# Performance work log

Measured on AMD Instinct MI355X. Metric: run time of the kernel, lower is better.

Reference implementation:

```python
import jax, jax.numpy as jnp
import numpy as np
import math

B, S, D = 2, 1024, 1024
H = 16
HD = D // H
E = 8
DFF = 4096
EPS = 1e-5


def _ln(x, g, b):
    m = jnp.mean(x, axis=-1, keepdims=True)
    v = jnp.mean((x - m) ** 2, axis=-1, keepdims=True)
    return (x - m) / jnp.sqrt(v + EPS) * g + b


def setup_inputs() -> dict:
    key = jax.random.key(0)
    ks = jax.random.split(key, 16)
    s = 0.02
    inp = {
        'src': jax.random.normal(ks[0], (B, S, D), jnp.float32),
        'qw': jax.random.normal(ks[1], (D, D), jnp.float32) * s,
        'kw': jax.random.normal(ks[2], (D, D), jnp.float32) * s,
        'vw': jax.random.normal(ks[3], (D, D), jnp.float32) * s,
        'ow': jax.random.normal(ks[4], (D, D), jnp.float32) * s,
        'gate_w': jax.random.normal(ks[5], (D, D), jnp.float32) * s,
        'gate_b': jax.random.normal(ks[6], (D,), jnp.float32) * s,
        'scale_w': jax.random.normal(ks[7], (H, HD), jnp.float32) * s,
        'n1_g': jnp.ones((D,), jnp.float32),
        'n1_b': jnp.zeros((D,), jnp.float32),
        'n2_g': jnp.ones((D,), jnp.float32),
        'n2_b': jnp.zeros((D,), jnp.float32),
        'moe_gate_w': jax.random.normal(ks[8], (D, E), jnp.float32) * s,
        'moe_gate_b': jnp.zeros((E,), jnp.float32),
        'w1': jax.random.normal(ks[9], (E, D, DFF), jnp.float32) * s,
        'b1': jnp.zeros((E, DFF), jnp.float32),
        'ln_g': jnp.ones((E, DFF), jnp.float32),
        'ln_b': jnp.zeros((E, DFF), jnp.float32),
        'w2': jax.random.normal(ks[10], (E, DFF, D), jnp.float32) * s,
        'b2': jnp.zeros((E, D), jnp.float32),
        'res_scale': jnp.ones((E,), jnp.float32),
    }
    return inp


def _forward(src, qw, kw, vw, ow, gate_w, gate_b, scale_w, n1_g, n1_b, n2_g, n2_b,
             moe_gate_w, moe_gate_b, w1, b1, ln_g, ln_b, w2, b2, res_scale):
    # ---- MemoAttention (non-flash path, eval: no dropout, no mask) ----
    q = (src @ qw).reshape(B, S, H, HD).transpose(0, 2, 1, 3)  # [B,H,S,HD]
    k = (src @ kw).reshape(B, S, H, HD).transpose(0, 2, 1, 3)
    v = (src @ vw).reshape(B, S, H, HD).transpose(0, 2, 1, 3)
    scores = jnp.einsum('bhqd,bhkd->bhqk', q, k) / math.sqrt(HD)
    # dynamic per-(head,query) scale gate
    scale = jax.nn.sigmoid(jnp.einsum('bhsd,hd->bhs', q, scale_w)) * 2.0
    scores = scores * scale[..., None]
    attn = jax.nn.softmax(scores, axis=-1)
    out = jnp.einsum('bhqk,bhkd->bhqd', attn, v)
    out = out.transpose(0, 2, 1, 3).reshape(B, S, D)
    gate = jax.nn.sigmoid(out @ gate_w + gate_b)
    attn_out = (out * gate) @ ow

    x = _ln(src + attn_out, n1_g, n1_b)

    # ---- MoE FFN (top-2 routing; eval: no gate noise; capacity never exceeded) ----
    xf = x.reshape(-1, D)                      # [T, D]
    T = xf.shape[0]
    logits = xf @ moe_gate_w + moe_gate_b      # [T, E]
    top_v, top_i = jax.lax.top_k(logits, 2)
    # NB: original sums BOTH top-k softmax weights per token (== 1.0), and the
    wsum = jnp.sum(jax.nn.softmax(top_v, axis=-1), axis=-1)   # [T] (== 1)
    e_sel = jnp.max(top_i, axis=-1)                           # [T]
    # dense per-expert FFN on all tokens, then per-token select (masked compute)
    h = jnp.einsum('td,edf->etf', xf, w1) + b1[:, None, :]    # [E,T,DFF]
    h = _ln(h, ln_g[:, None, :], ln_b[:, None, :])
    h = jax.nn.gelu(h, approximate=False)                     # torch nn.GELU (erf)
    y = jnp.einsum('etf,efd->etd', h, w2) + b2[:, None, :]    # [E,T,D]
    y = y * res_scale[:, None, None] + xf[None]
    sel = jnp.take_along_axis(y, e_sel[None, :, None], axis=0)[0]  # [T,D]
    moe_out = (sel * wsum[:, None]).reshape(B, S, D)

    return _ln(x + moe_out, n2_g, n2_b)


def reference(src, qw, kw, vw, ow, gate_w, gate_b, scale_w, n1_g, n1_b, n2_g, n2_b,
              moe_gate_w, moe_gate_b, w1, b1, ln_g, ln_b, w2, b2, res_scale):
    return _forward(src, qw, kw, vw, ow, gate_w, gate_b, scale_w, n1_g, n1_b,
                    n2_g, n2_b, moe_gate_w, moe_gate_b, w1, b1, ln_g, ln_b,
                    w2, b2, res_scale)
```

## Files before the change

### kernel.cpp

```cpp
#include <hip/hip_runtime.h>
#include <math.h>

#define TOK    2048
#define DMODEL 1024
#define NHEAD  16
#define HDIM   64
#define NEXP   8
#define DFFN   4096

typedef unsigned short u16;
typedef __attribute__((ext_vector_type(8))) short short8;
typedef __attribute__((ext_vector_type(4))) float floatx4;

__device__ __forceinline__ float sigmoidf_(float x) { return 1.f / (1.f + __expf(-x)); }

__device__ __forceinline__ u16 f2bf(float f) {
  union { float f; unsigned u; } v; v.f = f;
  unsigned r = v.u + 0x7FFFu + ((v.u >> 16) & 1u);
  return (u16)(r >> 16);
}
__device__ __forceinline__ float bf2f(u16 h) {
  union { unsigned u; float f; } v; v.u = ((unsigned)h) << 16; return v.f;
}

__device__ __forceinline__ void gload16(const void* g, void* l) {
  __builtin_amdgcn_global_load_lds((const __attribute__((address_space(1))) void*)g,
                                   (__attribute__((address_space(3))) void*)l, 16, 0, 0);
}

__device__ __forceinline__ float blockReduceSum256(float val) {
  __shared__ float ws_[4];
  #pragma unroll
  for (int off = 32; off; off >>= 1) val += __shfl_down(val, off);
  int lane = threadIdx.x & 63, w = threadIdx.x >> 6;
  if (lane == 0) ws_[w] = val;
  __syncthreads();
  float r = ws_[0] + ws_[1] + ws_[2] + ws_[3];
  __syncthreads();
  return r;
}

__global__ __launch_bounds__(256) void split_kernel(
    const float* __restrict__ X, u16* __restrict__ Hi, u16* __restrict__ Lo) {
  const int i = blockIdx.x * 256 + threadIdx.x;
  const float4 v = ((const float4*)X)[i];
  const float f[4] = {v.x, v.y, v.z, v.w};
  union { u16 s[4]; uint2 u; } h, l;
  #pragma unroll
  for (int j = 0; j < 4; ++j) {
    h.s[j] = f2bf(f[j]);
    l.s[j] = f2bf(f[j] - bf2f(h.s[j]));
  }
  ((uint2*)Hi)[i] = h.u;
  ((uint2*)Lo)[i] = l.u;
}

template<bool LO>
__global__ __launch_bounds__(256) void wt_conv_kernel(
    const float* __restrict__ W, u16* __restrict__ Whi, u16* __restrict__ Wlo,
    int K, int N) {
  const size_t z = blockIdx.z;
  W   += z * (size_t)K * N;
  Whi += z * (size_t)K * N;
  if (LO) Wlo += z * (size_t)K * N;
  __shared__ float tile[32][33];
  const int n0 = blockIdx.x * 32, k0 = blockIdx.y * 32;
  const int r = threadIdx.x >> 3, c4 = (threadIdx.x & 7) * 4;
  const float4 v = *(const float4*)&W[(size_t)(k0 + r) * N + n0 + c4];
  tile[r][c4+0] = v.x; tile[r][c4+1] = v.y; tile[r][c4+2] = v.z; tile[r][c4+3] = v.w;
  __syncthreads();
  union { u16 s[4]; uint2 u; } h, l;
  #pragma unroll
  for (int j = 0; j < 4; ++j) {
    const float f = tile[c4 + j][r];
    h.s[j] = f2bf(f);
    if (LO) l.s[j] = f2bf(f - bf2f(h.s[j]));
  }
  *(uint2*)&Whi[(size_t)(n0 + r) * K + k0 + c4] = h.u;
  if (LO) *(uint2*)&Wlo[(size_t)(n0 + r) * K + k0 + c4] = l.u;
}

__global__ __launch_bounds__(256) void wt3_conv_kernel(
    const float* __restrict__ Q, const float* __restrict__ Kw,
    const float* __restrict__ V, u16* __restrict__ Whi, u16* __restrict__ Wlo) {
  const int zz = blockIdx.z >> 5;
  const float* W = (zz == 0) ? Q : (zz == 1) ? Kw : V;
  u16* Whi_ = Whi + (size_t)zz * DMODEL * DMODEL;
  u16* Wlo_ = Wlo + (size_t)zz * DMODEL * DMODEL;
  __shared__ float tile[32][33];
  const int n0 = blockIdx.x * 32, k0 = (blockIdx.z & 31) * 32;
  const int r = threadIdx.x >> 3, c4 = (threadIdx.x & 7) * 4;
  const float4 v = *(const float4*)&W[(size_t)(k0 + r) * DMODEL + n0 + c4];
  tile[r][c4+0] = v.x; tile[r][c4+1] = v.y; tile[r][c4+2] = v.z; tile[r][c4+3] = v.w;
  __syncthreads();
  union { u16 s[4]; uint2 u; } h, l;
  #pragma unroll
  for (int j = 0; j < 4; ++j) {
    const float f = tile[c4 + j][r];
    h.s[j] = f2bf(f);
    l.s[j] = f2bf(f - bf2f(h.s[j]));
  }
  *(uint2*)&Whi_[(size_t)(n0 + r) * DMODEL + k0 + c4] = h.u;
  *(uint2*)&Wlo_[(size_t)(n0 + r) * DMODEL + k0 + c4] = l.u;
}

template<int EPI, int TN>
__global__ __launch_bounds__(256, TN == 64 ? 3 : 2) void gemm_split_kernel(
    const u16* __restrict__ Ahi, const u16* __restrict__ Alo,
    const u16* __restrict__ Whi, const u16* __restrict__ Wlo,
    const float* __restrict__ bias, const float* __restrict__ mul,
    float* __restrict__ Cf, u16* __restrict__ Chi, u16* __restrict__ Clo,
    u16* __restrict__ Vth, u16* __restrict__ Vtl,
    int M, int N, int K) {
  constexpr int NF = TN / 32;
  __shared__ u16 Ah[128*64], Al[128*64], Bh[TN*64], Bl[TN*64];
  const int tid = threadIdx.x;
  const int lane = tid & 63, wave = tid >> 6;
  const int row0 = blockIdx.y * 128, col0 = blockIdx.x * TN;
  const int wm = (wave & 1) * 64, wn = (wave >> 1) * (TN / 2);
  const int mr = tid >> 3;
  const int ksrc = (tid & 7) ^ ((tid >> 3) & 7);
  const floatx4 zero = {0.f, 0.f, 0.f, 0.f};
  floatx4 acc[4][NF];
  #pragma unroll
  for (int i = 0; i < 4; ++i)
    #pragma unroll
    for (int j = 0; j < NF; ++j) acc[i][j] = zero;

  for (int k0 = 0; k0 < K; k0 += 64) {
    __syncthreads();
    #pragma unroll
    for (int p = 0; p < 4; ++p) {
      const size_t ga = (size_t)(row0 + p * 32 + mr) * K + (k0 + ksrc * 8);
      const size_t off = (size_t)(p * 256 + wave * 64) * 16;
      gload16(Ahi + ga, (char*)Ah + off);
      gload16(Alo + ga, (char*)Al + off);
    }
    #pragma unroll
    for (int p = 0; p < NF; ++p) {
      const size_t gb = (size_t)(col0 + p * 32 + mr) * K + (k0 + ksrc * 8);
      const size_t off = (size_t)(p * 256 + wave * 64) * 16;
      gload16(Whi + gb, (char*)Bh + off);
      gload16(Wlo + gb, (char*)Bl + off);
    }
    __syncthreads();
    #pragma unroll
    for (int kk = 0; kk < 2; ++kk) {
      short8 ah[4], al[4], bh[NF], bl[NF];
      #pragma unroll
      for (int i = 0; i < 4; ++i) {
        const int ml = wm + i * 16 + (lane & 15);
        const int cm = (kk * 4 + (lane >> 4)) ^ (ml & 7);
        ah[i] = *(const short8*)&Ah[ml * 64 + cm * 8];
        al[i] = *(const short8*)&Al[ml * 64 + cm * 8];
      }
      #pragma unroll
      for (int j = 0; j < NF; ++j) {
        const int nl = wn + j * 16 + (lane & 15);
        const int cn = (kk * 4 + (lane >> 4)) ^ (nl & 7);
        bh[j] = *(const short8*)&Bh[nl * 64 + cn * 8];
        bl[j] = *(const short8*)&Bl[nl * 64 + cn * 8];
      }
      #pragma unroll
      for (int i = 0; i < 4; ++i)
        #pragma unroll
        for (int j = 0; j < NF; ++j) {
          acc[i][j] = __builtin_amdgcn_mfma_f32_16x16x32_bf16(ah[i], bh[j], acc[i][j], 0, 0, 0);
          acc[i][j] = __builtin_amdgcn_mfma_f32_16x16x32_bf16(al[i], bh[j], acc[i][j], 0, 0, 0);
          acc[i][j] = __builtin_amdgcn_mfma_f32_16x16x32_bf16(ah[i], bl[j], acc[i][j], 0, 0, 0);
        }
    }
  }
  const int cl = lane & 15, quad = lane >> 4;
  if (EPI == 2 && col0 >= 2048) {
    #pragma unroll
    for (int i = 0; i < 4; ++i)
      #pragma unroll
      for (int j = 0; j < NF; ++j) {
        const int dg = col0 + wn + j * 16 + cl - 2048;
        const int bh_ = dg >> 6, d = dg & 63;
        const int row = row0 + wm + i * 16 + quad * 4;
        const int b = row >> 10, t0 = row & 1023;
        union { u16 s[4]; uint2 u; } hh, ll;
        #pragma unroll
        for (int r = 0; r < 4; ++r) {
          const float v = acc[i][j][r];
          hh.s[r] = f2bf(v);
          ll.s[r] = f2bf(v - bf2f(hh.s[r]));
        }
        const size_t base = ((size_t)(b * 16 + bh_) * 64 + d) * 1024 + t0;
        *(uint2*)&Vth[base] = hh.u;
        *(uint2*)&Vtl[base] = ll.u;
      }
    return;
  }
  #pragma unroll
  for (int i = 0; i < 4; ++i)
    #pragma unroll
    for (int j = 0; j < NF; ++j) {
      const int col = col0 + wn + j * 16 + cl;
      #pragma unroll
      for (int r = 0; r < 4; ++r) {
        const int row = row0 + wm + i * 16 + quad * 4 + r;
        const float v = acc[i][j][r];
        if (EPI == 0) {
          Cf[(size_t)row * N + col] = v;
        } else if (EPI == 1) {
          const float s = sigmoidf_(v + bias[col]);
          const float g = s * mul[(size_t)row * N + col];
          const u16 hh = f2bf(g);
          Chi[(size_t)row * N + col] = hh;
          Clo[(size_t)row * N + col] = f2bf(g - bf2f(hh));
        } else {
          const u16 hh = f2bf(v);
          Chi[(size_t)row * N + col] = hh;
          Clo[(size_t)row * N + col] = f2bf(v - bf2f(hh));
        }
      }
    }
}

template<int EPI, int TN>
__global__ __launch_bounds__(256, TN == 64 ? 4 : 3) void gemm_moe_kernel(
    const u16* __restrict__ A, const u16* __restrict__ Wt,
    const float* __restrict__ bias,
    const int* __restrict__ perm, const int* __restrict__ offs,
    const int* __restrict__ counts,
    u16* __restrict__ Hout, float* __restrict__ P0, float* __restrict__ P1,
    int N, int K, int e_base) {
  constexpr int NF = TN / 32;
  const int z = blockIdx.z;
  const int ez = (EPI == 0) ? z : (z & 3);
  const int ks = (EPI == 0) ? 0 : (z >> 2);
  const int e = e_base + ez;
  const int ne = counts[e];
  const int tm = blockIdx.y;
  if (tm * 128 >= ne) return;
  const int kbeg = (EPI == 0) ? 0 : ks * (K >> 1);
  const int kend = (EPI == 0) ? K : kbeg + (K >> 1);
  __shared__ u16 As_[128*64], Bs_[TN*64];
  __shared__ int toks[128];
  const int tid = threadIdx.x;
  if (tid < 128) {
    const int idx = tm * 128 + tid;
    toks[tid] = perm[offs[e] + (idx < ne ? idx : 0)];
  }
  __syncthreads();
  const int lane = tid & 63, wave = tid >> 6;
  const int wm = (wave & 1) * 64, wn = (wave >> 1) * (TN / 2);
  const int mr = tid >> 3;
  const int ksrc = (tid & 7) ^ ((tid >> 3) & 7);
  size_t abase[4];
  #pragma unroll
  for (int p = 0; p < 4; ++p) abase[p] = (size_t)toks[p * 32 + mr] * K;
  const u16* We = Wt + (size_t)ez * N * K;
  const int col0 = blockIdx.x * TN;
  const floatx4 zero = {0.f, 0.f, 0.f, 0.f};
  floatx4 acc[4][NF];
  #pragma unroll
  for (int i = 0; i < 4; ++i)
    #pragma unroll
    for (int j = 0; j < NF; ++j) acc[i][j] = zero;

  for (int k0 = kbeg; k0 < kend; k0 += 64) {
    __syncthreads();
    #pragma unroll
    for (int p = 0; p < 4; ++p) {
      const size_t off = (size_t)(p * 256 + wave * 64) * 16;
      gload16(A + abase[p] + (k0 + ksrc * 8), (char*)As_ + off);
    }
    #pragma unroll
    for (int p = 0; p < NF; ++p) {
      const size_t off = (size_t)(p * 256 + wave * 64) * 16;
      gload16(We + (size_t)(col0 + p * 32 + mr) * K + (k0 + ksrc * 8), (char*)Bs_ + off);
    }
    __syncthreads();
    #pragma unroll
    for (int kk = 0; kk < 2; ++kk) {
      short8 a[4], b[NF];
      #pragma unroll
      for (int i = 0; i < 4; ++i) {
        const int ml = wm + i * 16 + (lane & 15);
        const int cm = (kk * 4 + (lane >> 4)) ^ (ml & 7);
        a[i] = *(const short8*)&As_[ml * 64 + cm * 8];
      }
      #pragma unroll
      for (int j = 0; j < NF; ++j) {
        const int nl = wn + j * 16 + (lane & 15);
        const int cn = (kk * 4 + (lane >> 4)) ^ (nl & 7);
        b[j] = *(const short8*)&Bs_[nl * 64 + cn * 8];
      }
      #pragma unroll
      for (int i = 0; i < 4; ++i)
        #pragma unroll
        for (int j = 0; j < NF; ++j)
          acc[i][j] = __builtin_amdgcn_mfma_f32_16x16x32_bf16(a[i], b[j], acc[i][j], 0, 0, 0);
    }
  }
  const int cl = lane & 15, quad = lane >> 4;
  float* Pp = (EPI == 1) ? (ks ? P1 : P0) : nullptr;
  #pragma unroll
  for (int i = 0; i < 4; ++i)
    #pragma unroll
    for (int j = 0; j < NF; ++j) {
      const int col = col0 + wn + j * 16 + cl;
      #pragma unroll
      for (int r = 0; r < 4; ++r) {
        const int rl = wm + i * 16 + quad * 4 + r;
        if (tm * 128 + rl < ne) {
          const int tok = toks[rl];
          if (EPI == 0)
            Hout[(size_t)tok * N + col] = f2bf(acc[i][j][r] + bias[(size_t)e * N + col]);
          else
            Pp[(size_t)tok * N + col] = acc[i][j][r];
        }
      }
    }
}

__global__ __launch_bounds__(512, 2) void attn_mfma_kernel(
    const u16* __restrict__ QKh, const u16* __restrict__ QKl,
    const u16* __restrict__ Vth, const u16* __restrict__ Vtl,
    const float* __restrict__ scale_w,
    float* __restrict__ AOf, u16* __restrict__ AOh, u16* __restrict__ AOl) {
  const int qt = blockIdx.x, h = blockIdx.y, b = blockIdx.z;
  __shared__ u16 Kh[64*64], Kl[64*64], Vh[64*64], Vl[64*64];
  __shared__ u16 Ph[8][16*40], Pl[8][16*40];
  const int tid = threadIdx.x, lane = tid & 63, wave = tid >> 6;
  const int i15 = lane & 15, quad = lane >> 4;
  const floatx4 zero = {0.f, 0.f, 0.f, 0.f};

  short8 qh[2], ql[2];
  const size_t qrow = ((size_t)b * 1024 + qt * 128 + wave * 16 + i15) * 3072 + h * 64;
  #pragma unroll
  for (int kk = 0; kk < 2; ++kk) {
    qh[kk] = *(const short8*)&QKh[qrow + kk * 32 + quad * 8];
    ql[kk] = *(const short8*)&QKl[qrow + kk * 32 + quad * 8];
  }
  float dot = 0.f;
  #pragma unroll
  for (int kk = 0; kk < 2; ++kk)
    #pragma unroll
    for (int j = 0; j < 8; ++j) {
      const float sw = scale_w[h * 64 + kk * 32 + quad * 8 + j];
      dot += (bf2f((u16)qh[kk][j]) + bf2f((u16)ql[kk][j])) * sw;
    }
  dot += __shfl_xor(dot, 16);
  dot += __shfl_xor(dot, 32);
  const float g = 2.f * sigmoidf_(dot) * 0.125f;
  float stot[4];
  #pragma unroll
  for (int r = 0; r < 4; ++r) stot[r] = __shfl(g, (lane >> 4) * 4 + r);

  float m_r[4], l_r[4];
  floatx4 Of[4];
  #pragma unroll
  for (int r = 0; r < 4; ++r) { m_r[r] = -1e30f; l_r[r] = 0.f; }
  #pragma unroll
  for (int f = 0; f < 4; ++f) Of[f] = zero;
  u16* PhW = Ph[wave];
  u16* PlW = Pl[wave];

  const int sr = tid >> 3;
  const int sc = ((tid & 7) ^ (sr & 7)) * 8;
  for (int kt = 0; kt < 16; ++kt) {
    __syncthreads();
    {
      const size_t off = (size_t)wave * 1024;
      const size_t kg = ((size_t)b * 1024 + kt * 64 + sr) * 3072 + 1024 + h * 64 + sc;
      gload16(QKh + kg, (char*)Kh + off);
      gload16(QKl + kg, (char*)Kl + off);
      const size_t vg = ((size_t)(b * 16 + h) * 64 + sr) * 1024 + kt * 64 + sc;
      gload16(Vth + vg, (char*)Vh + off);
      gload16(Vtl + vg, (char*)Vl + off);
    }
    __syncthreads();
    float pm[4][4];
    #pragma unroll
    for (int jn = 0; jn < 4; ++jn) {
      floatx4 a = zero;
      #pragma unroll
      for (int kk = 0; kk < 2; ++kk) {
        const int n = jn * 16 + i15;
        const int ch = ((kk * 4 + quad) ^ (n & 7)) * 8;
        const short8 bh = *(const short8*)&Kh[n * 64 + ch];
        const short8 bl = *(const short8*)&Kl[n * 64 + ch];
        a = __builtin_amdgcn_mfma_f32_16x16x32_bf16(qh[kk], bh, a, 0, 0, 0);
        a = __builtin_amdgcn_mfma_f32_16x16x32_bf16(ql[kk], bh, a, 0, 0, 0);
        a = __builtin_amdgcn_mfma_f32_16x16x32_bf16(qh[kk], bl, a, 0, 0, 0);
      }
      #pragma unroll
      for (int r = 0; r < 4; ++r) pm[jn][r] = a[r] * stot[r];
    }
    float alpha[4];
    #pragma unroll
    for (int r = 0; r < 4; ++r) {
      float mx = fmaxf(fmaxf(pm[0][r], pm[1][r]), fmaxf(pm[2][r], pm[3][r]));
      mx = fmaxf(mx, __shfl_xor(mx, 1));
      mx = fmaxf(mx, __shfl_xor(mx, 2));
      mx = fmaxf(mx, __shfl_xor(mx, 4));
      mx = fmaxf(mx, __shfl_xor(mx, 8));
      const float mn = fmaxf(m_r[r], mx);
      alpha[r] = __expf(m_r[r] - mn);
      m_r[r] = mn;
      float rs = 0.f;
      #pragma unroll
      for (int jn = 0; jn < 4; ++jn) { pm[jn][r] = __expf(pm[jn][r] - mn); rs += pm[jn][r]; }
      rs += __shfl_xor(rs, 1);
      rs += __shfl_xor(rs, 2);
      rs += __shfl_xor(rs, 4);
      rs += __shfl_xor(rs, 8);
      l_r[r] = l_r[r] * alpha[r] + rs;
    }
    #pragma unroll
    for (int f = 0; f < 4; ++f)
      #pragma unroll
      for (int r = 0; r < 4; ++r) Of[f][r] *= alpha[r];
    #pragma unroll
    for (int kk = 0; kk < 2; ++kk) {
      #pragma unroll
      for (int jj = 0; jj < 2; ++jj) {
        const int jn = kk * 2 + jj;
        #pragma unroll
        for (int r = 0; r < 4; ++r) {
          const int a = (quad * 4 + r) * 40 + jj * 16 + i15;
          const u16 hh = f2bf(pm[jn][r]);
          PhW[a] = hh;
          PlW[a] = f2bf(pm[jn][r] - bf2f(hh));
        }
      }
      const short8 pah = *(const short8*)&PhW[i15 * 40 + quad * 8];
      const short8 pal = *(const short8*)&PlW[i15 * 40 + quad * 8];
      #pragma unroll
      for (int f = 0; f < 4; ++f) {
        const int d = f * 16 + i15;
        const int ch = ((kk * 4 + quad) ^ (d & 7)) * 8;
        const short8 vbh = *(const short8*)&Vh[d * 64 + ch];
        const short8 vbl = *(const short8*)&Vl[d * 64 + ch];
        Of[f] = __builtin_amdgcn_mfma_f32_16x16x32_bf16(pah, vbh, Of[f], 0, 0, 0);
        Of[f] = __builtin_amdgcn_mfma_f32_16x16x32_bf16(pal, vbh, Of[f], 0, 0, 0);
        Of[f] = __builtin_amdgcn_mfma_f32_16x16x32_bf16(pah, vbl, Of[f], 0, 0, 0);
      }
    }
  }
  float inv[4];
  #pragma unroll
  for (int r = 0; r < 4; ++r) inv[r] = 1.f / l_r[r];
  #pragma unroll
  for (int f = 0; f < 4; ++f)
    #pragma unroll
    for (int r = 0; r < 4; ++r) {
      const size_t row = (size_t)b * 1024 + qt * 128 + wave * 16 + quad * 4 + r;
      const int col = h * 64 + f * 16 + i15;
      const float val = Of[f][r] * inv[r];
      AOf[row * 1024 + col] = val;
      const u16 hh = f2bf(val);
      AOh[row * 1024 + col] = hh;
      AOl[row * 1024 + col] = f2bf(val - bf2f(hh));
    }
}

template<bool BF>
__global__ __launch_bounds__(256) void ln_add_kernel(
    const float* __restrict__ A, const float* __restrict__ Bp,
    const float* __restrict__ g, const float* __restrict__ beta,
    float* __restrict__ outf, u16* __restrict__ outh) {
  int t = blockIdx.x, tid = threadIdx.x;
  const float* a = A + (size_t)t * DMODEL;
  const float* b = Bp + (size_t)t * DMODEL;
  float v[4]; float s = 0.f;
  #pragma unroll
  for (int i = 0; i < 4; ++i) { int d = tid + i*256; v[i] = a[d] + b[d]; s += v[i]; }
  s = blockReduceSum256(s);
  float mean = s * (1.f/1024.f);
  float q = 0.f;
  #pragma unroll
  for (int i = 0; i < 4; ++i) { float df = v[i]-mean; q += df*df; }
  q = blockReduceSum256(q);
  float rstd = rsqrtf(q*(1.f/1024.f) + 1e-5f);
  #pragma unroll
  for (int i = 0; i < 4; ++i) {
    int d = tid + i*256;
    float val = (v[i]-mean)*rstd*g[d] + beta[d];
    outf[(size_t)t*DMODEL + d] = val;
    if (BF) outh[(size_t)t*DMODEL + d] = f2bf(val);
  }
}

__global__ __launch_bounds__(256) void ln_final_kernel(
    const float* __restrict__ X, const float* __restrict__ P0,
    const float* __restrict__ P1, const float* __restrict__ B2,
    const float* __restrict__ rsv, const int* __restrict__ e_sel,
    const float* __restrict__ g, const float* __restrict__ beta,
    float* __restrict__ out) {
  int t = blockIdx.x, tid = threadIdx.x;
  const int e = e_sel[t];
  const float rse = rsv[e];
  const float* b2e = B2 + (size_t)e * DMODEL;
  const int d0 = tid * 4;
  const size_t base = (size_t)t * DMODEL + d0;
  const float4 xv = *(const float4*)&X[base];
  const float4 p0v = *(const float4*)&P0[base];
  const float4 p1v = *(const float4*)&P1[base];
  const float4 bv = *(const float4*)&b2e[d0];
  float v[4]; float s = 0.f;
  v[0] = 2.f*xv.x + (p0v.x + p1v.x + bv.x) * rse;
  v[1] = 2.f*xv.y + (p0v.y + p1v.y + bv.y) * rse;
  v[2] = 2.f*xv.z + (p0v.z + p1v.z + bv.z) * rse;
  v[3] = 2.f*xv.w + (p0v.w + p1v.w + bv.w) * rse;
  s = v[0] + v[1] + v[2] + v[3];
  s = blockReduceSum256(s);
  float mean = s * (1.f/1024.f);
  float q = 0.f;
  #pragma unroll
  for (int i = 0; i < 4; ++i) { float df = v[i]-mean; q += df*df; }
  q = blockReduceSum256(q);
  float rstd = rsqrtf(q*(1.f/1024.f) + 1e-5f);
  const float4 g4 = *(const float4*)&g[d0];
  const float4 be4 = *(const float4*)&beta[d0];
  float4 o;
  o.x = (v[0]-mean)*rstd*g4.x + be4.x;
  o.y = (v[1]-mean)*rstd*g4.y + be4.y;
  o.z = (v[2]-mean)*rstd*g4.z + be4.z;
  o.w = (v[3]-mean)*rstd*g4.w + be4.w;
  *(float4*)&out[base] = o;
}

__global__ __launch_bounds__(256) void moe_gate_kernel(
    const float* __restrict__ X, const float* __restrict__ gw,
    const float* __restrict__ gb, int* __restrict__ e_sel) {
  int wave = threadIdx.x >> 6, lane = threadIdx.x & 63;
  int token = blockIdx.x * 4 + wave;
  const float* x = X + (size_t)token * DMODEL;
  float acc[NEXP] = {};
  for (int d = lane; d < DMODEL; d += 64) {
    float xv = x[d];
    const float* gr = gw + (size_t)d * NEXP;
    #pragma unroll
    for (int e = 0; e < NEXP; ++e) acc[e] += xv * gr[e];
  }
  #pragma unroll
  for (int e = 0; e < NEXP; ++e) {
    #pragma unroll
    for (int off = 32; off; off >>= 1) acc[e] += __shfl_down(acc[e], off);
  }
  if (lane == 0) {
    float lg[NEXP];
    #pragma unroll
    for (int e = 0; e < NEXP; ++e) lg[e] = acc[e] + gb[e];
    int i1 = 0;
    for (int e = 1; e < NEXP; ++e) if (lg[e] > lg[i1]) i1 = e;
    int i2 = -1;
    for (int e = 0; e < NEXP; ++e) {
      if (e == i1) continue;
      if (i2 < 0 || lg[e] > lg[i2]) i2 = e;
    }
    e_sel[token] = (i1 > i2) ? i1 : i2;
  }
}

__global__ __launch_bounds__(256) void moe_group_kernel(
    const int* __restrict__ e_sel, int* __restrict__ perm,
    int* __restrict__ g_offs, int* __restrict__ g_counts) {
  __shared__ int cnt[NEXP], offs[NEXP], cur[NEXP];
  int tid = threadIdx.x;
  if (tid < NEXP) cnt[tid] = 0;
  __syncthreads();
  for (int t = tid; t < TOK; t += 256) atomicAdd(&cnt[e_sel[t]], 1);
  __syncthreads();
  if (tid == 0) {
    int run = 0;
    for (int e = 0; e < NEXP; ++e) { offs[e] = run; cur[e] = run; run += cnt[e]; }
  }
  __syncthreads();
  if (tid < NEXP) { g_offs[tid] = offs[tid]; g_counts[tid] = cnt[tid]; }
  for (int t = tid; t < TOK; t += 256) {
    int pos = atomicAdd(&cur[e_sel[t]], 1);
    perm[pos] = t;
  }
}

__global__ __launch_bounds__(256) void moe_ln_gelu_kernel(
    u16* __restrict__ H, const float* __restrict__ ln_g,
    const float* __restrict__ ln_b, const int* __restrict__ e_sel) {
  int t = blockIdx.x, tid = threadIdx.x;
  int e = e_sel[t];
  u16* hp = H + (size_t)t * DFFN;
  float v[16]; float s = 0.f;
  #pragma unroll
  for (int i = 0; i < 4; ++i) {
    const int d = i * 1024 + tid * 4;
    union { uint2 u; u16 q[4]; } hv;
    hv.u = *(const uint2*)&hp[d];
    #pragma unroll
    for (int j = 0; j < 4; ++j) { v[i*4+j] = bf2f(hv.q[j]); s += v[i*4+j]; }
  }
  s = blockReduceSum256(s);
  float mean = s * (1.f/4096.f);
  float q = 0.f;
  #pragma unroll
  for (int i = 0; i < 16; ++i) { float df = v[i]-mean; q += df*df; }
  q = blockReduceSum256(q);
  float rstd = rsqrtf(q*(1.f/4096.f) + 1e-5f);
  const float* gg = ln_g + (size_t)e * DFFN;
  const float* bb = ln_b + (size_t)e * DFFN;
  #pragma unroll
  for (int i = 0; i < 4; ++i) {
    const int d = i * 1024 + tid * 4;
    const float4 g4 = *(const float4*)&gg[d];
    const float4 b4 = *(const float4*)&bb[d];
    const float gf[4] = {g4.x, g4.y, g4.z, g4.w};
    const float bf[4] = {b4.x, b4.y, b4.z, b4.w};
    union { uint2 u; u16 q[4]; } ov;
    #pragma unroll
    for (int j = 0; j < 4; ++j) {
      float xx = (v[i*4+j]-mean)*rstd*gf[j] + bf[j];
      ov.q[j] = f2bf(0.5f * xx * (1.f + erff(xx * 0.7071067811865475f)));
    }
    *(uint2*)&hp[d] = ov.u;
  }
}

extern "C" void kernel_launch(void* const* d_in, const int* in_sizes, int n_in,
                              void* d_out, int out_size, void* d_ws, size_t ws_size,
                              hipStream_t stream) {
  (void)in_sizes; (void)n_in; (void)out_size; (void)ws_size;
  const float* src    = (const float*)d_in[0];
  const float* qw     = (const float*)d_in[1];
  const float* kw     = (const float*)d_in[2];
  const float* vw     = (const float*)d_in[3];
  const float* ow     = (const float*)d_in[4];
  const float* gate_w = (const float*)d_in[5];
  const float* gate_b = (const float*)d_in[6];
  const float* scale_w= (const float*)d_in[7];
  const float* n1_g   = (const float*)d_in[8];
  const float* n1_b   = (const float*)d_in[9];
  const float* n2_g   = (const float*)d_in[10];
  const float* n2_b   = (const float*)d_in[11];
  const float* mgw    = (const float*)d_in[12];
  const float* mgb    = (const float*)d_in[13];
  const float* w1     = (const float*)d_in[14];
  const float* b1     = (const float*)d_in[15];
  const float* ln_g   = (const float*)d_in[16];
  const float* ln_b   = (const float*)d_in[17];
  const float* w2     = (const float*)d_in[18];
  const float* b2     = (const float*)d_in[19];
  const float* rs     = (const float*)d_in[20];

  char* ws = (char*)d_ws;
  const size_t MB = 1024 * 1024;
  u16*   qkv_hi = (u16*)(ws + 0*MB);
  u16*   qkv_lo = (u16*)(ws + 12*MB);
  u16*   Wt3_hi = (u16*)(ws + 24*MB);
  u16*   Wt3_lo = (u16*)(ws + 30*MB);
  u16*   Vt_hi  = (u16*)(ws + 36*MB);
  u16*   Vt_lo  = (u16*)(ws + 40*MB);
  u16*   src_hi = (u16*)(ws + 44*MB);
  u16*   src_lo = (u16*)(ws + 48*MB);
  float* ao     = (float*)(ws + 44*MB);
  u16*   ao_hi  = (u16*)(ws + 52*MB);
  u16*   ao_lo  = (u16*)(ws + 56*MB);
  u16*   gb_hi  = (u16*)(ws + 60*MB);
  u16*   gb_lo  = (u16*)(ws + 64*MB);
  float* proj   = (float*)(ws + 0*MB);
  float* x      = (float*)(ws + 8*MB);
  u16*   x_hi   = (u16*)(ws + 16*MB);
  u16*   WtA    = (u16*)(ws + 24*MB);
  u16*   h      = (u16*)(ws + 56*MB);
  float* p0     = (float*)(ws + 0*MB);
  float* p1     = (float*)(ws + 72*MB);
  int*   e_sel  = (int*)(ws + 80*MB);
  int*   perm   = e_sel + TOK;
  int*   offs   = perm + TOK;
  int*   cnts   = offs + NEXP;

  dim3 blk(256);
  split_kernel<<<2048, blk, 0, stream>>>(src, src_hi, src_lo);

  wt3_conv_kernel<<<dim3(32,1,96), blk, 0, stream>>>(qw, kw, vw, Wt3_hi, Wt3_lo);
  gemm_split_kernel<2,64><<<dim3(48,16), blk, 0, stream>>>(src_hi, src_lo, Wt3_hi, Wt3_lo,
      nullptr, nullptr, nullptr, qkv_hi, qkv_lo, Vt_hi, Vt_lo, TOK, 3072, DMODEL);

  attn_mfma_kernel<<<dim3(8, NHEAD, 2), dim3(512), 0, stream>>>(
      qkv_hi, qkv_lo, Vt_hi, Vt_lo, scale_w, ao, ao_hi, ao_lo);

  wt_conv_kernel<true><<<dim3(32,32,1), blk, 0, stream>>>(gate_w, Wt3_hi, Wt3_lo, DMODEL, DMODEL);
  gemm_split_kernel<1,64><<<dim3(16,16), blk, 0, stream>>>(ao_hi, ao_lo, Wt3_hi, Wt3_lo,
      gate_b, ao, nullptr, gb_hi, gb_lo, nullptr, nullptr, TOK, DMODEL, DMODEL);
  wt_conv_kernel<true><<<dim3(32,32,1), blk, 0, stream>>>(ow, Wt3_hi, Wt3_lo, DMODEL, DMODEL);
  gemm_split_kernel<0,64><<<dim3(16,16), blk, 0, stream>>>(gb_hi, gb_lo, Wt3_hi, Wt3_lo,
      nullptr, nullptr, proj, nullptr, nullptr, nullptr, nullptr, TOK, DMODEL, DMODEL);

  ln_add_kernel<true><<<TOK, blk, 0, stream>>>(src, proj, n1_g, n1_b, x, x_hi);

  moe_gate_kernel<<<TOK/4, blk, 0, stream>>>(x, mgw, mgb, e_sel);
  moe_group_kernel<<<1, blk, 0, stream>>>(e_sel, perm, offs, cnts);

  for (int c = 0; c < 2; ++c) {
    wt_conv_kernel<false><<<dim3(DFFN/32, DMODEL/32, 4), blk, 0, stream>>>(
        w1 + (size_t)c*4*DMODEL*DFFN, WtA, nullptr, DMODEL, DFFN);
    gemm_moe_kernel<0,128><<<dim3(DFFN/128, 16, 4), blk, 0, stream>>>(
        x_hi, WtA, b1, perm, offs, cnts, h, nullptr, nullptr, DFFN, DMODEL, c*4);
  }
  moe_ln_gelu_kernel<<<TOK, blk, 0, stream>>>(h, ln_g, ln_b, e_sel);
  for (int c = 0; c < 2; ++c) {
    wt_conv_kernel<false><<<dim3(DMODEL/32, DFFN/32, 4), blk, 0, stream>>>(
        w2 + (size_t)c*4*DFFN*DMODEL, WtA, nullptr, DFFN, DMODEL);
    gemm_moe_kernel<1,64><<<dim3(DMODEL/64, 16, 8), blk, 0, stream>>>(
        h, WtA, nullptr, perm, offs, cnts, nullptr, p0, p1, DMODEL, DFFN, c*4);
  }
  ln_final_kernel<<<TOK, blk, 0, stream>>>(x, p0, p1, b2, rs, e_sel, n2_g, n2_b, (float*)d_out);
}
```

Measured before the change: 713.7 us.

## Overlap MoE weight conversion with attention and projection GEMMs via fused launches

Folds the MoE w1 and w2 fp32-to-bf16 transpose conversions into the attention and gate/output-projection kernels as extra blocks, so the weight-bandwidth-heavy conversion runs concurrently with compute-bound work. All preprocessing of src and the dense weights is merged into one prep kernel, and the router is fused into the LayerNorm-add kernel. The expert GEMMs now run as single launches over all eight experts using full-size converted weight buffers. This needs a much larger workspace, and the fused kernels mix heterogeneous blocks, which can unbalance scheduling and raise shared-memory use through the unions.

```diff
diff --git a/kernel.cpp b/kernel.cpp
--- a/kernel.cpp
+++ b/kernel.cpp
@@ -40,56 +40,45 @@
   return r;
 }
 
-__global__ __launch_bounds__(256) void split_kernel(
-    const float* __restrict__ X, u16* __restrict__ Hi, u16* __restrict__ Lo) {
-  const int i = blockIdx.x * 256 + threadIdx.x;
-  const float4 v = ((const float4*)X)[i];
-  const float f[4] = {v.x, v.y, v.z, v.w};
-  union { u16 s[4]; uint2 u; } h, l;
-  #pragma unroll
-  for (int j = 0; j < 4; ++j) {
-    h.s[j] = f2bf(f[j]);
-    l.s[j] = f2bf(f[j] - bf2f(h.s[j]));
-  }
-  ((uint2*)Hi)[i] = h.u;
-  ((uint2*)Lo)[i] = l.u;
-}
-
-template<bool LO>
-__global__ __launch_bounds__(256) void wt_conv_kernel(
-    const float* __restrict__ W, u16* __restrict__ Whi, u16* __restrict__ Wlo,
-    int K, int N) {
-  const size_t z = blockIdx.z;
-  W   += z * (size_t)K * N;
-  Whi += z * (size_t)K * N;
-  if (LO) Wlo += z * (size_t)K * N;
+__global__ __launch_bounds__(256) void prep_kernel(
+    const float* __restrict__ src, u16* __restrict__ Shi, u16* __restrict__ Slo,
+    const float* __restrict__ Qw, const float* __restrict__ Kw, const float* __restrict__ Vw,
+    u16* __restrict__ W3h, u16* __restrict__ W3l,
+    const float* __restrict__ Gw, u16* __restrict__ Gh, u16* __restrict__ Gl,
+    const float* __restrict__ Ow, u16* __restrict__ Oh, u16* __restrict__ Ol) {
+  const int bid = blockIdx.x, tid = threadIdx.x;
   __shared__ float tile[32][33];
-  const int n0 = blockIdx.x * 32, k0 = blockIdx.y * 32;
-  const int r = threadIdx.x >> 3, c4 = (threadIdx.x & 7) * 4;
-  const float4 v = *(const float4*)&W[(size_t)(k0 + r) * N + n0 + c4];
-  tile[r][c4+0] = v.x; tile[r][c4+1] = v.y; tile[r][c4+2] = v.z; tile[r][c4+3] = v.w;
-  __syncthreads();
-  union { u16 s[4]; uint2 u; } h, l;
-  #pragma unroll
-  for (int j = 0; j < 4; ++j) {
-    const float f = tile[c4 + j][r];
-    h.s[j] = f2bf(f);
-    if (LO) l.s[j] = f2bf(f - bf2f(h.s[j]));
-  }
-  *(uint2*)&Whi[(size_t)(n0 + r) * K + k0 + c4] = h.u;
-  if (LO) *(uint2*)&Wlo[(size_t)(n0 + r) * K + k0 + c4] = l.u;
-}
-
-__global__ __launch_bounds__(256) void wt3_conv_kernel(
-    const float* __restrict__ Q, const float* __restrict__ Kw,
-    const float* __restrict__ V, u16* __restrict__ Whi, u16* __restrict__ Wlo) {
-  const int zz = blockIdx.z >> 5;
-  const float* W = (zz == 0) ? Q : (zz == 1) ? Kw : V;
-  u16* Whi_ = Whi + (size_t)zz * DMODEL * DMODEL;
-  u16* Wlo_ = Wlo + (size_t)zz * DMODEL * DMODEL;
-  __shared__ float tile[32][33];
-  const int n0 = blockIdx.x * 32, k0 = (blockIdx.z & 31) * 32;
-  const int r = threadIdx.x >> 3, c4 = (threadIdx.x & 7) * 4;
+  if (bid < 2048) {
+    const int i = bid * 256 + tid;
+    const float4 v = ((const float4*)src)[i];
+    const float f[4] = {v.x, v.y, v.z, v.w};
+    union { u16 s[4]; uint2 u; } h, l;
+    #pragma unroll
+    for (int j = 0; j < 4; ++j) {
+      h.s[j] = f2bf(f[j]);
+      l.s[j] = f2bf(f[j] - bf2f(h.s[j]));
+    }
+    ((uint2*)Shi)[i] = h.u;
+    ((uint2*)Slo)[i] = l.u;
+    return;
+  }
+  const float* W; u16 *Whp, *Wlp; int n0, k0, ldk;
+  if (bid < 5120) {
+    const int t = bid - 2048;
+    const int z = t >> 5;
+    const int zz = z >> 5;
+    W = (zz == 0) ? Qw : (zz == 1) ? Kw : Vw;
+    Whp = W3h + (size_t)zz * DMODEL * DMODEL;
+    Wlp = W3l + (size_t)zz * DMODEL * DMODEL;
+    n0 = (t & 31) * 32; k0 = (z & 31) * 32; ldk = DMODEL;
+  } else {
+    const int t = bid - 5120;
+    const int t2 = t & 1023;
+    if (t < 1024) { W = Gw; Whp = Gh; Wlp = Gl; }
+    else          { W = Ow; Whp = Oh; Wlp = Ol; }
+    n0 = (t2 & 31) * 32; k0 = (t2 >> 5) * 32; ldk = DMODEL;
+  }
+  const int r = tid >> 3, c4 = (tid & 7) * 4;
   const float4 v = *(const float4*)&W[(size_t)(k0 + r) * DMODEL + n0 + c4];
   tile[r][c4+0] = v.x; tile[r][c4+1] = v.y; tile[r][c4+2] = v.z; tile[r][c4+3] = v.w;
   __syncthreads();
@@ -100,12 +89,13 @@
     h.s[j] = f2bf(f);
     l.s[j] = f2bf(f - bf2f(h.s[j]));
   }
-  *(uint2*)&Whi_[(size_t)(n0 + r) * DMODEL + k0 + c4] = h.u;
-  *(uint2*)&Wlo_[(size_t)(n0 + r) * DMODEL + k0 + c4] = l.u;
+  *(uint2*)&Whp[(size_t)(n0 + r) * ldk + k0 + c4] = h.u;
+  *(uint2*)&Wlp[(size_t)(n0 + r) * ldk + k0 + c4] = l.u;
 }
 
 template<int EPI, int TN>
-__global__ __launch_bounds__(256, TN == 64 ? 3 : 2) void gemm_split_kernel(
+__device__ __forceinline__ void gemm_split_body(
+    u16* Ah, u16* Al, u16* Bh, u16* Bl, int bx, int by,
     const u16* __restrict__ Ahi, const u16* __restrict__ Alo,
     const u16* __restrict__ Whi, const u16* __restrict__ Wlo,
     const float* __restrict__ bias, const float* __restrict__ mul,
@@ -113,10 +103,9 @@
     u16* __restrict__ Vth, u16* __restrict__ Vtl,
     int M, int N, int K) {
   constexpr int NF = TN / 32;
-  __shared__ u16 Ah[128*64], Al[128*64], Bh[TN*64], Bl[TN*64];
   const int tid = threadIdx.x;
   const int lane = tid & 63, wave = tid >> 6;
-  const int row0 = blockIdx.y * 128, col0 = blockIdx.x * TN;
+  const int row0 = by * 128, col0 = bx * TN;
   const int wm = (wave & 1) * 64, wn = (wave >> 1) * (TN / 2);
   const int mr = tid >> 3;
   const int ksrc = (tid & 7) ^ ((tid >> 3) & 7);
@@ -221,18 +210,65 @@
 }
 
 template<int EPI, int TN>
+__global__ __launch_bounds__(256, TN == 64 ? 3 : 2) void gemm_split_kernel(
+    const u16* __restrict__ Ahi, const u16* __restrict__ Alo,
+    const u16* __restrict__ Whi, const u16* __restrict__ Wlo,
+    const float* __restrict__ bias, const float* __restrict__ mul,
+    float* __restrict__ Cf, u16* __restrict__ Chi, u16* __restrict__ Clo,
+    u16* __restrict__ Vth, u16* __restrict__ Vtl,
+    int M, int N, int K) {
+  __shared__ u16 Ah[128*64], Al[128*64], Bh[TN*64], Bl[TN*64];
+  gemm_split_body<EPI, TN>(Ah, Al, Bh, Bl, blockIdx.x, blockIdx.y,
+      Ahi, Alo, Whi, Wlo, bias, mul, Cf, Chi, Clo, Vth, Vtl, M, N, K);
+}
+
+struct GemmShared { u16 Ah[128*64]; u16 Al[128*64]; u16 Bh[64*64]; u16 Bl[64*64]; };
+template<int EPI>
+__global__ __launch_bounds__(256, 3) void gemm_split_w2_kernel(
+    const u16* __restrict__ Ahi, const u16* __restrict__ Alo,
+    const u16* __restrict__ Whi, const u16* __restrict__ Wlo,
+    const float* __restrict__ bias, const float* __restrict__ mul,
+    float* __restrict__ Cf, u16* __restrict__ Chi, u16* __restrict__ Clo,
+    const float* __restrict__ W2, u16* __restrict__ W2b, int khalf) {
+  __shared__ union { GemmShared g; float tile[32][33]; } sm;
+  const int bid = blockIdx.x;
+  if (bid < 256) {
+    gemm_split_body<EPI, 64>(sm.g.Ah, sm.g.Al, sm.g.Bh, sm.g.Bl, bid & 15, bid >> 4,
+        Ahi, Alo, Whi, Wlo, bias, mul, Cf, Chi, Clo, nullptr, nullptr,
+        TOK, DMODEL, DMODEL);
+    return;
+  }
+  const int t = bid - 256;
+  const int e = t >> 5, n0 = (t & 31) * 32;
+  const float* W = W2 + (size_t)e * DFFN * DMODEL;
+  u16* O = W2b + (size_t)e * DMODEL * DFFN;
+  const int r = threadIdx.x >> 3, c4 = (threadIdx.x & 7) * 4;
+  for (int kt = 0; kt < 64; ++kt) {
+    const int k0 = khalf * 2048 + kt * 32;
+    __syncthreads();
+    const float4 v = *(const float4*)&W[(size_t)(k0 + r) * DMODEL + n0 + c4];
+    sm.tile[r][c4+0] = v.x; sm.tile[r][c4+1] = v.y;
+    sm.tile[r][c4+2] = v.z; sm.tile[r][c4+3] = v.w;
+    __syncthreads();
+    union { u16 s[4]; uint2 u; } h4;
+    #pragma unroll
+    for (int j = 0; j < 4; ++j) h4.s[j] = f2bf(sm.tile[c4 + j][r]);
+    *(uint2*)&O[(size_t)(n0 + r) * DFFN + k0 + c4] = h4.u;
+  }
+}
+
+template<int EPI, int TN>
 __global__ __launch_bounds__(256, TN == 64 ? 4 : 3) void gemm_moe_kernel(
     const u16* __restrict__ A, const u16* __restrict__ Wt,
     const float* __restrict__ bias,
     const int* __restrict__ perm, const int* __restrict__ offs,
     const int* __restrict__ counts,
     u16* __restrict__ Hout, float* __restrict__ P0, float* __restrict__ P1,
-    int N, int K, int e_base) {
+    int N, int K) {
   constexpr int NF = TN / 32;
   const int z = blockIdx.z;
-  const int ez = (EPI == 0) ? z : (z & 3);
-  const int ks = (EPI == 0) ? 0 : (z >> 2);
-  const int e = e_base + ez;
+  const int e = (EPI == 0) ? z : (z & 7);
+  const int ks = (EPI == 0) ? 0 : (z >> 3);
   const int ne = counts[e];
   const int tm = blockIdx.y;
   if (tm * 128 >= ne) return;
@@ -253,7 +289,7 @@
   size_t abase[4];
   #pragma unroll
   for (int p = 0; p < 4; ++p) abase[p] = (size_t)toks[p * 32 + mr] * K;
-  const u16* We = Wt + (size_t)ez * N * K;
+  const u16* We = Wt + (size_t)e * N * K;
   const int col0 = blockIdx.x * TN;
   const floatx4 zero = {0.f, 0.f, 0.f, 0.f};
   floatx4 acc[4][NF];
@@ -318,15 +354,43 @@
     }
 }
 
-__global__ __launch_bounds__(512, 2) void attn_mfma_kernel(
+struct AttnShared {
+  u16 Kh[64*64], Kl[64*64], Vh[64*64], Vl[64*64];
+  u16 Ph[8][16*40], Pl[8][16*40];
+};
+__global__ __launch_bounds__(512, 2) void attn_w1conv_kernel(
     const u16* __restrict__ QKh, const u16* __restrict__ QKl,
     const u16* __restrict__ Vth, const u16* __restrict__ Vtl,
     const float* __restrict__ scale_w,
-    float* __restrict__ AOf, u16* __restrict__ AOh, u16* __restrict__ AOl) {
-  const int qt = blockIdx.x, h = blockIdx.y, b = blockIdx.z;
-  __shared__ u16 Kh[64*64], Kl[64*64], Vh[64*64], Vl[64*64];
-  __shared__ u16 Ph[8][16*40], Pl[8][16*40];
-  const int tid = threadIdx.x, lane = tid & 63, wave = tid >> 6;
+    float* __restrict__ AOf, u16* __restrict__ AOh, u16* __restrict__ AOl,
+    const float* __restrict__ W1, u16* __restrict__ W1b) {
+  __shared__ union { AttnShared a; float tile[64][65]; } sm;
+  const int bid = blockIdx.x;
+  const int tid = threadIdx.x;
+  if (bid >= 256) {
+    const int s = bid - 256;
+    const int e = s >> 6, n0 = (s & 63) * 64;
+    const float* W = W1 + (size_t)e * DMODEL * DFFN;
+    u16* O = W1b + (size_t)e * DFFN * DMODEL;
+    const int r = tid >> 3, c8 = (tid & 7) * 8;
+    for (int k0 = 0; k0 < DMODEL; k0 += 64) {
+      __syncthreads();
+      const float4 v0 = *(const float4*)&W[(size_t)(k0 + r) * DFFN + n0 + c8];
+      const float4 v1 = *(const float4*)&W[(size_t)(k0 + r) * DFFN + n0 + c8 + 4];
+      sm.tile[r][c8+0] = v0.x; sm.tile[r][c8+1] = v0.y;
+      sm.tile[r][c8+2] = v0.z; sm.tile[r][c8+3] = v0.w;
+      sm.tile[r][c8+4] = v1.x; sm.tile[r][c8+5] = v1.y;
+      sm.tile[r][c8+6] = v1.z; sm.tile[r][c8+7] = v1.w;
+      __syncthreads();
+      union { u16 s_[8]; uint4 u; } h8;
+      #pragma unroll
+      for (int j = 0; j < 8; ++j) h8.s_[j] = f2bf(sm.tile[c8 + j][r]);
+      *(uint4*)&O[(size_t)(n0 + r) * DMODEL + k0 + c8] = h8.u;
+    }
+    return;
+  }
+  const int qt = bid & 7, h = (bid >> 3) & 15, b = bid >> 7;
+  const int lane = tid & 63, wave = tid >> 6;
   const int i15 = lane & 15, quad = lane >> 4;
   const floatx4 zero = {0.f, 0.f, 0.f, 0.f};
 
@@ -358,8 +422,8 @@
   for (int r = 0; r < 4; ++r) { m_r[r] = -1e30f; l_r[r] = 0.f; }
   #pragma unroll
   for (int f = 0; f < 4; ++f) Of[f] = zero;
-  u16* PhW = Ph[wave];
-  u16* PlW = Pl[wave];
+  u16* PhW = sm.a.Ph[wave];
+  u16* PlW = sm.a.Pl[wave];
 
   const int sr = tid >> 3;
   const int sc = ((tid & 7) ^ (sr & 7)) * 8;
@@ -368,11 +432,11 @@
     {
       const size_t off = (size_t)wave * 1024;
       const size_t kg = ((size_t)b * 1024 + kt * 64 + sr) * 3072 + 1024 + h * 64 + sc;
-      gload16(QKh + kg, (char*)Kh + off);
-      gload16(QKl + kg, (char*)Kl + off);
+      gload16(QKh + kg, (char*)sm.a.Kh + off);
+      gload16(QKl + kg, (char*)sm.a.Kl + off);
       const size_t vg = ((size_t)(b * 16 + h) * 64 + sr) * 1024 + kt * 64 + sc;
-      gload16(Vth + vg, (char*)Vh + off);
-      gload16(Vtl + vg, (char*)Vl + off);
+      gload16(Vth + vg, (char*)sm.a.Vh + off);
+      gload16(Vtl + vg, (char*)sm.a.Vl + off);
     }
     __syncthreads();
     float pm[4][4];
@@ -383,8 +447,8 @@
       for (int kk = 0; kk < 2; ++kk) {
         const int n = jn * 16 + i15;
         const int ch = ((kk * 4 + quad) ^ (n & 7)) * 8;
-        const short8 bh = *(const short8*)&Kh[n * 64 + ch];
-        const short8 bl = *(const short8*)&Kl[n * 64 + ch];
+        const short8 bh = *(const short8*)&sm.a.Kh[n * 64 + ch];
+        const short8 bl = *(const short8*)&sm.a.Kl[n * 64 + ch];
         a = __builtin_amdgcn_mfma_f32_16x16x32_bf16(qh[kk], bh, a, 0, 0, 0);
         a = __builtin_amdgcn_mfma_f32_16x16x32_bf16(ql[kk], bh, a, 0, 0, 0);
         a = __builtin_amdgcn_mfma_f32_16x16x32_bf16(qh[kk], bl, a, 0, 0, 0);
@@ -435,8 +499,8 @@
       for (int f = 0; f < 4; ++f) {
         const int d = f * 16 + i15;
         const int ch = ((kk * 4 + quad) ^ (d & 7)) * 8;
-        const short8 vbh = *(const short8*)&Vh[d * 64 + ch];
-        const short8 vbl = *(const short8*)&Vl[d * 64 + ch];
+        const short8 vbh = *(const short8*)&sm.a.Vh[d * 64 + ch];
+        const short8 vbl = *(const short8*)&sm.a.Vl[d * 64 + ch];
         Of[f] = __builtin_amdgcn_mfma_f32_16x16x32_bf16(pah, vbh, Of[f], 0, 0, 0);
         Of[f] = __builtin_amdgcn_mfma_f32_16x16x32_bf16(pal, vbh, Of[f], 0, 0, 0);
         Of[f] = __builtin_amdgcn_mfma_f32_16x16x32_bf16(pah, vbl, Of[f], 0, 0, 0);
@@ -460,11 +524,13 @@
     }
 }
 
-template<bool BF>
-__global__ __launch_bounds__(256) void ln_add_kernel(
+__global__ __launch_bounds__(256) void ln_add_router_kernel(
     const float* __restrict__ A, const float* __restrict__ Bp,
     const float* __restrict__ g, const float* __restrict__ beta,
-    float* __restrict__ outf, u16* __restrict__ outh) {
+    float* __restrict__ outf, u16* __restrict__ outh,
+    const float* __restrict__ gw, const float* __restrict__ gb,
+    int* __restrict__ e_sel) {
+  __shared__ float xrow[DMODEL];
   int t = blockIdx.x, tid = threadIdx.x;
   const float* a = A + (size_t)t * DMODEL;
   const float* b = Bp + (size_t)t * DMODEL;
@@ -483,7 +549,36 @@
     int d = tid + i*256;
     float val = (v[i]-mean)*rstd*g[d] + beta[d];
     outf[(size_t)t*DMODEL + d] = val;
-    if (BF) outh[(size_t)t*DMODEL + d] = f2bf(val);
+    outh[(size_t)t*DMODEL + d] = f2bf(val);
+    xrow[d] = val;
+  }
+  __syncthreads();
+  if (tid < 64) {
+    float acc[NEXP] = {};
+    for (int d = tid; d < DMODEL; d += 64) {
+      float xv = xrow[d];
+      const float* gr = gw + (size_t)d * NEXP;
+      #pragma unroll
+      for (int e = 0; e < NEXP; ++e) acc[e] += xv * gr[e];
+    }
+    #pragma unroll
+    for (int e = 0; e < NEXP; ++e) {
+      #pragma unroll
+      for (int off = 32; off; off >>= 1) acc[e] += __shfl_down(acc[e], off);
+    }
+    if (tid == 0) {
+      float lg[NEXP];
+      #pragma unroll
+      for (int e = 0; e < NEXP; ++e) lg[e] = acc[e] + gb[e];
+      int i1 = 0;
+      for (int e = 1; e < NEXP; ++e) if (lg[e] > lg[i1]) i1 = e;
+      int i2 = -1;
+      for (int e = 0; e < NEXP; ++e) {
+        if (e == i1) continue;
+        if (i2 < 0 || lg[e] > lg[i2]) i2 = e;
+      }
+      e_sel[t] = (i1 > i2) ? i1 : i2;
+    }
   }
 }
 
@@ -526,39 +621,6 @@
   *(float4*)&out[base] = o;
 }
 
-__global__ __launch_bounds__(256) void moe_gate_kernel(
-    const float* __restrict__ X, const float* __restrict__ gw,
-    const float* __restrict__ gb, int* __restrict__ e_sel) {
-  int wave = threadIdx.x >> 6, lane = threadIdx.x & 63;
-  int token = blockIdx.x * 4 + wave;
-  const float* x = X + (size_t)token * DMODEL;
-  float acc[NEXP] = {};
-  for (int d = lane; d < DMODEL; d += 64) {
-    float xv = x[d];
-    const float* gr = gw + (size_t)d * NEXP;
-    #pragma unroll
-    for (int e = 0; e < NEXP; ++e) acc[e] += xv * gr[e];
-  }
-  #pragma unroll
-  for (int e = 0; e < NEXP; ++e) {
-    #pragma unroll
-    for (int off = 32; off; off >>= 1) acc[e] += __shfl_down(acc[e], off);
-  }
-  if (lane == 0) {
-    float lg[NEXP];
-    #pragma unroll
-    for (int e = 0; e < NEXP; ++e) lg[e] = acc[e] + gb[e];
-    int i1 = 0;
-    for (int e = 1; e < NEXP; ++e) if (lg[e] > lg[i1]) i1 = e;
-    int i2 = -1;
-    for (int e = 0; e < NEXP; ++e) {
-      if (e == i1) continue;
-      if (i2 < 0 || lg[e] > lg[i2]) i2 = e;
-    }
-    e_sel[token] = (i1 > i2) ? i1 : i2;
-  }
-}
-
 __global__ __launch_bounds__(256) void moe_group_kernel(
     const int* __restrict__ e_sel, int* __restrict__ perm,
     int* __restrict__ g_offs, int* __restrict__ g_counts) {
@@ -649,65 +711,67 @@
 
   char* ws = (char*)d_ws;
   const size_t MB = 1024 * 1024;
-  u16*   qkv_hi = (u16*)(ws + 0*MB);
-  u16*   qkv_lo = (u16*)(ws + 12*MB);
-  u16*   Wt3_hi = (u16*)(ws + 24*MB);
-  u16*   Wt3_lo = (u16*)(ws + 30*MB);
-  u16*   Vt_hi  = (u16*)(ws + 36*MB);
-  u16*   Vt_lo  = (u16*)(ws + 40*MB);
-  u16*   src_hi = (u16*)(ws + 44*MB);
-  u16*   src_lo = (u16*)(ws + 48*MB);
-  float* ao     = (float*)(ws + 44*MB);
-  u16*   ao_hi  = (u16*)(ws + 52*MB);
-  u16*   ao_lo  = (u16*)(ws + 56*MB);
-  u16*   gb_hi  = (u16*)(ws + 60*MB);
-  u16*   gb_lo  = (u16*)(ws + 64*MB);
-  float* proj   = (float*)(ws + 0*MB);
-  float* x      = (float*)(ws + 8*MB);
-  u16*   x_hi   = (u16*)(ws + 16*MB);
-  u16*   WtA    = (u16*)(ws + 24*MB);
-  u16*   h      = (u16*)(ws + 56*MB);
-  float* p0     = (float*)(ws + 0*MB);
-  float* p1     = (float*)(ws + 72*MB);
-  int*   e_sel  = (int*)(ws + 80*MB);
+  u16*   src_hi = (u16*)(ws + 0*MB);
+  u16*   src_lo = (u16*)(ws + 4*MB);
+  u16*   Wt3_hi = (u16*)(ws + 8*MB);
+  u16*   Wt3_lo = (u16*)(ws + 14*MB);
+  u16*   gw_hi  = (u16*)(ws + 20*MB);
+  u16*   gw_lo  = (u16*)(ws + 22*MB);
+  u16*   ow_hi  = (u16*)(ws + 24*MB);
+  u16*   ow_lo  = (u16*)(ws + 26*MB);
+  u16*   W1A    = (u16*)(ws + 28*MB);
+  u16*   W2A    = (u16*)(ws + 92*MB);
+  u16*   qkv_hi = (u16*)(ws + 156*MB);
+  u16*   qkv_lo = (u16*)(ws + 168*MB);
+  u16*   Vt_hi  = (u16*)(ws + 180*MB);
+  u16*   Vt_lo  = (u16*)(ws + 184*MB);
+  float* ao     = (float*)(ws + 188*MB);
+  u16*   ao_hi  = (u16*)(ws + 196*MB);
+  u16*   ao_lo  = (u16*)(ws + 200*MB);
+  u16*   gb_hi  = (u16*)(ws + 204*MB);
+  u16*   gb_lo  = (u16*)(ws + 208*MB);
+  float* proj   = (float*)(ws + 212*MB);
+  float* x      = (float*)(ws + 220*MB);
+  u16*   x_hi   = (u16*)(ws + 228*MB);
+  u16*   h      = (u16*)(ws + 232*MB);
+  float* p0     = (float*)(ws + 248*MB);
+  float* p1     = (float*)(ws + 256*MB);
+  int*   e_sel  = (int*)(ws + 264*MB);
   int*   perm   = e_sel + TOK;
   int*   offs   = perm + TOK;
   int*   cnts   = offs + NEXP;
 
   dim3 blk(256);
-  split_kernel<<<2048, blk, 0, stream>>>(src, src_hi, src_lo);
-
-  wt3_conv_kernel<<<dim3(32,1,96), blk, 0, stream>>>(qw, kw, vw, Wt3_hi, Wt3_lo);
-  gemm_split_kernel<2,64><<<dim3(48,16), blk, 0, stream>>>(src_hi, src_lo, Wt3_hi, Wt3_lo,
-      nullptr, nullptr, nullptr, qkv_hi, qkv_lo, Vt_hi, Vt_lo, TOK, 3072, DMODEL);
-
-  attn_mfma_kernel<<<dim3(8, NHEAD, 2), dim3(512), 0, stream>>>(
-      qkv_hi, qkv_lo, Vt_hi, Vt_lo, scale_w, ao, ao_hi, ao_lo);
-
-  wt_conv_kernel<true><<<dim3(32,32,1), blk, 0, stream>>>(gate_w, Wt3_hi, Wt3_lo, DMODEL, DMODEL);
-  gemm_split_kernel<1,64><<<dim3(16,16), blk, 0, stream>>>(ao_hi, ao_lo, Wt3_hi, Wt3_lo,
-      gate_b, ao, nullptr, gb_hi, gb_lo, nullptr, nullptr, TOK, DMODEL, DMODEL);
-  wt_conv_kernel<true><<<dim3(32,32,1), blk, 0, stream>>>(ow, Wt3_hi, Wt3_lo, DMODEL, DMODEL);
-  gemm_split_kernel<0,64><<<dim3(16,16), blk, 0, stream>>>(gb_hi, gb_lo, Wt3_hi, Wt3_lo,
-      nullptr, nullptr, proj, nullptr, nullptr, nullptr, nullptr, TOK, DMODEL, DMODEL);
-
-  ln_add_kernel<true><<<TOK, blk, 0, stream>>>(src, proj, n1_g, n1_b, x, x_hi);
-
-  moe_gate_kernel<<<TOK/4, blk, 0, stream>>>(x, mgw, mgb, e_sel);
+
+  prep_kernel<<<7168, blk, 0, stream>>>(src, src_hi, src_lo,
+      qw, kw, vw, Wt3_hi, Wt3_lo, gate_w, gw_hi, gw_lo, ow, ow_hi, ow_lo);
+
+  gemm_split_kernel<2,64><<<dim3(48,16), blk, 0, stream>>>(src_hi, src_lo,
+      Wt3_hi, Wt3_lo, nullptr, nullptr, nullptr, qkv_hi, qkv_lo, Vt_hi, Vt_lo,
+      TOK, 3072, DMODEL);
+
+  attn_w1conv_kernel<<<768, dim3(512), 0, stream>>>(
+      qkv_hi, qkv_lo, Vt_hi, Vt_lo, scale_w, ao, ao_hi, ao_lo, w1, W1A);
+
+  gemm_split_w2_kernel<1><<<512, blk, 0, stream>>>(ao_hi, ao_lo, gw_hi, gw_lo,
+      gate_b, ao, nullptr, gb_hi, gb_lo, w2, W2A, 0);
+
+  gemm_split_w2_kernel<0><<<512, blk, 0, stream>>>(gb_hi, gb_lo, ow_hi, ow_lo,
+      nullptr, nullptr, proj, nullptr, nullptr, w2, W2A, 1);
+
+  ln_add_router_kernel<<<TOK, blk, 0, stream>>>(src, proj, n1_g, n1_b, x, x_hi,
+      mgw, mgb, e_sel);
+
   moe_group_kernel<<<1, blk, 0, stream>>>(e_sel, perm, offs, cnts);
 
-  for (int c = 0; c < 2; ++c) {
-    wt_conv_kernel<false><<<dim3(DFFN/32, DMODEL/32, 4), blk, 0, stream>>>(
-        w1 + (size_t)c*4*DMODEL*DFFN, WtA, nullptr, DMODEL, DFFN);
-    gemm_moe_kernel<0,128><<<dim3(DFFN/128, 16, 4), blk, 0, stream>>>(
-        x_hi, WtA, b1, perm, offs, cnts, h, nullptr, nullptr, DFFN, DMODEL, c*4);
-  }
+  gemm_moe_kernel<0,128><<<dim3(DFFN/128, 16, 8), blk, 0, stream>>>(
+      x_hi, W1A, b1, perm, offs, cnts, h, nullptr, nullptr, DFFN, DMODEL);
+
   moe_ln_gelu_kernel<<<TOK, blk, 0, stream>>>(h, ln_g, ln_b, e_sel);
-  for (int c = 0; c < 2; ++c) {
-    wt_conv_kernel<false><<<dim3(DMODEL/32, DFFN/32, 4), blk, 0, stream>>>(
-        w2 + (size_t)c*4*DFFN*DMODEL, WtA, nullptr, DFFN, DMODEL);
-    gemm_moe_kernel<1,64><<<dim3(DMODEL/64, 16, 8), blk, 0, stream>>>(
-        h, WtA, nullptr, perm, offs, cnts, nullptr, p0, p1, DMODEL, DFFN, c*4);
-  }
-  ln_final_kernel<<<TOK, blk, 0, stream>>>(x, p0, p1, b2, rs, e_sel, n2_g, n2_b, (float*)d_out);
-}
+
+  gemm_moe_kernel<1,64><<<dim3(DMODEL/64, 16, 16), blk, 0, stream>>>(
+      h, W2A, nullptr, perm, offs, cnts, nullptr, p0, p1, DMODEL, DFFN);
+
+  ln_final_kernel<<<TOK, blk, 0, stream>>>(x, p0, p1, b2, rs, e_sel, n2_g, n2_b,
+      (float*)d_out);
+}
```

New measurement: 740.6 us. 1.04x slower.
